# Kernel optimization log

Hardware: AMD Instinct MI355X
Metric: run time of the kernel (lower is better)

## Reference

```python
import jax, jax.numpy as jnp
import numpy as np

N, E, D = 40000, 640000, 128
BN_EPS = 1e-5


def setup_inputs() -> dict:
    key = jax.random.key(0)
    ks = jax.random.split(key, 6)
    x = jax.random.normal(ks[0], (N, D), dtype=jnp.float32)
    src = jax.random.randint(ks[1], (E,), 0, N, dtype=jnp.int64)
    dst = jax.random.randint(ks[2], (E,), 0, N, dtype=jnp.int64)
    W1 = jax.random.normal(ks[3], (D, D), dtype=jnp.float32) * (1.0 / np.sqrt(D))
    b1 = jnp.zeros((D,), dtype=jnp.float32)
    gamma = jnp.ones((D,), dtype=jnp.float32)
    beta = jnp.zeros((D,), dtype=jnp.float32)
    W2 = jax.random.normal(ks[4], (D, D), dtype=jnp.float32) * (1.0 / np.sqrt(D))
    b2 = jnp.zeros((D,), dtype=jnp.float32)
    eps = jnp.zeros((1,), dtype=jnp.float32)
    return {"x": x, "src": src, "dst": dst, "W1": W1, "b1": b1,
            "gamma": gamma, "beta": beta, "W2": W2, "b2": b2, "eps": eps}


def reference(x, src, dst, W1, b1, gamma, beta, W2, b2, eps):
    # edge gather + ReLU + scatter-sum aggregation  (copy_u -> relu -> sum)
    m = jax.nn.relu(x[src])                                  # [E, D]
    agg = jax.ops.segment_sum(m, dst, num_segments=N)        # [N, D]
    h = (1.0 + eps[0]) * x + agg                             # eps-scaled residual
    # MLP: Linear -> BatchNorm1d (batch stats) -> ReLU -> Linear
    h = h @ W1.T + b1
    mu = jnp.mean(h, axis=0)
    var = jnp.var(h, axis=0)                                 # biased, as torch BN
    h = (h - mu) * jax.lax.rsqrt(var + BN_EPS) * gamma + beta
    h = jax.nn.relu(h)
    return h @ W2.T + b2
```

## Files before the change

kernel.cpp:

```cpp
#include <hip/hip_runtime.h>

#define NN 40000
#define NE 640000
#define DD 128
#define CAP 64
#define NREP 8
#define NBLK 625
#define PA_BLOCKS 512
#define EPB (NE / PA_BLOCKS)
#define NBUCK 256
#define NODES_PB 157
#define CELL 32

typedef __attribute__((ext_vector_type(8))) short short8;
typedef __attribute__((ext_vector_type(4))) float floatx4;

__device__ __forceinline__ unsigned short f2bf(float f) {
    union { float f; unsigned u; } v; v.f = f;
    return (unsigned short)((v.u + 0x7fffu + ((v.u >> 16) & 1u)) >> 16);
}
__device__ __forceinline__ float bflo2f(unsigned u) {
    union { unsigned u; float f; } v; v.u = u << 16; return v.f;
}
__device__ __forceinline__ float bfhi2f(unsigned u) {
    union { unsigned u; float f; } v; v.u = u & 0xffff0000u; return v.f;
}


__global__ void k_passA(const int* __restrict__ src, const int* __restrict__ dst,
                        const float* __restrict__ x, const float* __restrict__ W1,
                        const float* __restrict__ W2, unsigned* __restrict__ part,
                        unsigned char* __restrict__ cntAB, unsigned short* __restrict__ xb,
                        unsigned short* __restrict__ W1b, unsigned short* __restrict__ W2b,
                        float* __restrict__ stats) {
    __shared__ unsigned hist[NBUCK];
    const int t = threadIdx.x, k = blockIdx.x;
    if (k == 0) {
        float4 z = {0.f, 0.f, 0.f, 0.f};
        ((float4*)stats)[t * 2] = z;
        ((float4*)stats)[t * 2 + 1] = z;
    }
    if (t < NBUCK) hist[t] = 0;
    __syncthreads();
    const int base = k * EPB;
    unsigned* myWin = part + ((unsigned)k << 8) * CELL;
    for (int i = t; i < EPB; i += 256) {
        int sv = src[base + i];
        int d  = dst[base + i];
        unsigned b = (unsigned)d / NODES_PB;
        unsigned slot = atomicAdd(&hist[b], 1u);
        if (slot < CELL)
            myWin[b * CELL + slot] =
                ((unsigned)(d - (int)(b * NODES_PB)) << 16) | (unsigned)sv;
    }
    __syncthreads();
    if (t < NBUCK) {
        unsigned c = hist[t];
        cntAB[k * NBUCK + t] = (unsigned char)(c < CELL ? c : CELL);
    }
    const int tid = k * 256 + t;
    const int P = PA_BLOCKS * 256;
    const float4* x4 = (const float4*)x;
    for (int i = tid; i < NN * DD / 4; i += P) {
        float4 v = x4[i];
        ushort4 o;
        o.x = f2bf(v.x); o.y = f2bf(v.y); o.z = f2bf(v.z); o.w = f2bf(v.w);
        ((ushort4*)xb)[i] = o;
    }
    if (tid < 8192) {
        const float4* w4 = (tid < 4096) ? (const float4*)W1 : (const float4*)W2;
        unsigned short* wb = (tid < 4096) ? W1b : W2b;
        int i = tid & 4095;
        float4 v = w4[i];
        ushort4 o;
        o.x = f2bf(v.x); o.y = f2bf(v.y); o.z = f2bf(v.z); o.w = f2bf(v.w);
        ((ushort4*)wb)[i] = o;
    }
}

__launch_bounds__(256)
__global__ void k_passB(const unsigned* __restrict__ part,
                        const unsigned char* __restrict__ cntAB,
                        int* __restrict__ cnt, unsigned short* __restrict__ eidx) {
    __shared__ unsigned lcnt[NODES_PB];
    __shared__ __align__(16) unsigned short llist[NODES_PB][CAP];
    const int g = blockIdx.x;
    const int t = threadIdx.x;
    const int n0 = g * NODES_PB;
    const int nCnt = (NN - n0 < NODES_PB) ? (NN - n0) : NODES_PB;
    if (t < NODES_PB) lcnt[t] = 0;
    __syncthreads();
    for (int k = t; k < PA_BLOCKS; k += 256) {
        int c = cntAB[k * NBUCK + g];
        const unsigned* cell = part + (((unsigned)k << 8) | (unsigned)g) * CELL;
        for (int i = 0; i < c; ++i) {
            unsigned e = cell[i];
            unsigned d = e >> 16;
            unsigned slot = atomicAdd(&lcnt[d], 1u);
            if (slot < CAP) llist[d][slot] = (unsigned short)(e & 0xffffu);
        }
    }
    __syncthreads();
    if (t < nCnt) cnt[n0 + t] = (int)lcnt[t];
    for (int idx = t; idx < nCnt * 8; idx += 256) {
        int row = idx >> 3, c = idx & 7;
        unsigned lc = lcnt[row]; lc = (lc > CAP) ? CAP : lc;
        if ((unsigned)c * 8 < lc)
            ((uint4*)eidx)[(unsigned)(n0 + row) * 8 + c] = *(const uint4*)&llist[row][c * 8];
    }
}

__launch_bounds__(256)
__global__ void k_gather(const unsigned short* __restrict__ xb,
                         const unsigned short* __restrict__ eidx,
                         const int* __restrict__ cnt, const float* __restrict__ eps,
                         unsigned short* __restrict__ h) {
    const int n = blockIdx.x * 4 + (threadIdx.x >> 6);
    const int lane = threadIdx.x & 63;
    const int half = lane >> 5, hl = lane & 31;
    const float s = 1.0f + eps[0];
    const uint2* xq = (const uint2*)xb;
    int deg = cnt[n];
    deg = (deg > CAP) ? CAP : deg;
    float f0, f1, f2, f3;
    {
        uint2 xv = xq[n * 32 + hl];
        float sm = (half == 0) ? s : 0.f;
        f0 = bflo2f(xv.x) * sm; f1 = bfhi2f(xv.x) * sm;
        f2 = bflo2f(xv.y) * sm; f3 = bfhi2f(xv.y) * sm;
    }
    const unsigned short* row = eidx + n * CAP;
    int j = 0;
    for (; j + 15 < deg; j += 16) {
        int e0 = row[j + half],      e1 = row[j + 2 + half];
        int e2 = row[j + 4 + half],  e3 = row[j + 6 + half];
        int e4 = row[j + 8 + half],  e5 = row[j + 10 + half];
        int e6 = row[j + 12 + half], e7 = row[j + 14 + half];
        uint2 v0 = xq[e0 * 32 + hl];
        uint2 v1 = xq[e1 * 32 + hl];
        uint2 v2 = xq[e2 * 32 + hl];
        uint2 v3 = xq[e3 * 32 + hl];
        uint2 v4 = xq[e4 * 32 + hl];
        uint2 v5 = xq[e5 * 32 + hl];
        uint2 v6 = xq[e6 * 32 + hl];
        uint2 v7 = xq[e7 * 32 + hl];
        f0 += ((fmaxf(bflo2f(v0.x), 0.f) + fmaxf(bflo2f(v1.x), 0.f)) +
               (fmaxf(bflo2f(v2.x), 0.f) + fmaxf(bflo2f(v3.x), 0.f))) +
              ((fmaxf(bflo2f(v4.x), 0.f) + fmaxf(bflo2f(v5.x), 0.f)) +
               (fmaxf(bflo2f(v6.x), 0.f) + fmaxf(bflo2f(v7.x), 0.f)));
        f1 += ((fmaxf(bfhi2f(v0.x), 0.f) + fmaxf(bfhi2f(v1.x), 0.f)) +
               (fmaxf(bfhi2f(v2.x), 0.f) + fmaxf(bfhi2f(v3.x), 0.f))) +
              ((fmaxf(bfhi2f(v4.x), 0.f) + fmaxf(bfhi2f(v5.x), 0.f)) +
               (fmaxf(bfhi2f(v6.x), 0.f) + fmaxf(bfhi2f(v7.x), 0.f)));
        f2 += ((fmaxf(bflo2f(v0.y), 0.f) + fmaxf(bflo2f(v1.y), 0.f)) +
               (fmaxf(bflo2f(v2.y), 0.f) + fmaxf(bflo2f(v3.y), 0.f))) +
              ((fmaxf(bflo2f(v4.y), 0.f) + fmaxf(bflo2f(v5.y), 0.f)) +
               (fmaxf(bflo2f(v6.y), 0.f) + fmaxf(bflo2f(v7.y), 0.f)));
        f3 += ((fmaxf(bfhi2f(v0.y), 0.f) + fmaxf(bfhi2f(v1.y), 0.f)) +
               (fmaxf(bfhi2f(v2.y), 0.f) + fmaxf(bfhi2f(v3.y), 0.f))) +
              ((fmaxf(bfhi2f(v4.y), 0.f) + fmaxf(bfhi2f(v5.y), 0.f)) +
               (fmaxf(bfhi2f(v6.y), 0.f) + fmaxf(bfhi2f(v7.y), 0.f)));
    }
    for (; j + 7 < deg; j += 8) {
        int e0 = row[j + half],     e1 = row[j + 2 + half];
        int e2 = row[j + 4 + half], e3 = row[j + 6 + half];
        uint2 v0 = xq[e0 * 32 + hl];
        uint2 v1 = xq[e1 * 32 + hl];
        uint2 v2 = xq[e2 * 32 + hl];
        uint2 v3 = xq[e3 * 32 + hl];
        f0 += (fmaxf(bflo2f(v0.x), 0.f) + fmaxf(bflo2f(v1.x), 0.f)) +
              (fmaxf(bflo2f(v2.x), 0.f) + fmaxf(bflo2f(v3.x), 0.f));
        f1 += (fmaxf(bfhi2f(v0.x), 0.f) + fmaxf(bfhi2f(v1.x), 0.f)) +
              (fmaxf(bfhi2f(v2.x), 0.f) + fmaxf(bfhi2f(v3.x), 0.f));
        f2 += (fmaxf(bflo2f(v0.y), 0.f) + fmaxf(bflo2f(v1.y), 0.f)) +
              (fmaxf(bflo2f(v2.y), 0.f) + fmaxf(bflo2f(v3.y), 0.f));
        f3 += (fmaxf(bfhi2f(v0.y), 0.f) + fmaxf(bfhi2f(v1.y), 0.f)) +
              (fmaxf(bfhi2f(v2.y), 0.f) + fmaxf(bfhi2f(v3.y), 0.f));
    }
    for (; j + 1 < deg; j += 2) {
        int e = row[j + half];
        uint2 v = xq[e * 32 + hl];
        f0 += fmaxf(bflo2f(v.x), 0.f); f1 += fmaxf(bfhi2f(v.x), 0.f);
        f2 += fmaxf(bflo2f(v.y), 0.f); f3 += fmaxf(bfhi2f(v.y), 0.f);
    }
    if (j < deg && half == 0) {
        int e = row[j];
        uint2 v = xq[e * 32 + hl];
        f0 += fmaxf(bflo2f(v.x), 0.f); f1 += fmaxf(bfhi2f(v.x), 0.f);
        f2 += fmaxf(bflo2f(v.y), 0.f); f3 += fmaxf(bfhi2f(v.y), 0.f);
    }
    f0 += __shfl_xor(f0, 32); f1 += __shfl_xor(f1, 32);
    f2 += __shfl_xor(f2, 32); f3 += __shfl_xor(f3, 32);
    if (half == 0) {
        unsigned lo = ((unsigned)f2bf(f1) << 16) | (unsigned)f2bf(f0);
        unsigned hi = ((unsigned)f2bf(f3) << 16) | (unsigned)f2bf(f2);
        ((uint2*)h)[n * 32 + hl] = make_uint2(lo, hi);
    }
}

__launch_bounds__(256)
__global__ void k_gg1(const unsigned short* __restrict__ h,
                      const unsigned short* __restrict__ W1b, const float* __restrict__ b1,
                      unsigned short* __restrict__ h1b, float* __restrict__ stats) {
    __shared__ __align__(16) unsigned short hbuf[64][DD + 8];
    __shared__ float red[2][4][DD];
    const int t = threadIdx.x;
    const int wv = t >> 6, lane = t & 63, m = lane & 15, q = lane >> 4;
    const int r0 = blockIdx.x * 64 + wv * 16;
    floatx4 acc[8];
    #pragma unroll
    for (int nt = 0; nt < 8; ++nt) acc[nt] = (floatx4){0.f, 0.f, 0.f, 0.f};
    {
        const unsigned short* arow = h + (r0 + m) * DD + q * 8;
        const unsigned short* brow = W1b + m * DD + q * 8;
        #pragma unroll
        for (int kt = 0; kt < 4; ++kt) {
            short8 a = *(const short8*)(arow + kt * 32);
            #pragma unroll
            for (int nt = 0; nt < 8; ++nt) {
                short8 b = *(const short8*)(brow + nt * 16 * DD + kt * 32);
                acc[nt] = __builtin_amdgcn_mfma_f32_16x16x32_bf16(a, b, acc[nt], 0, 0, 0);
            }
        }
    }
    #pragma unroll
    for (int nt = 0; nt < 8; ++nt) {
        float bv = b1[nt * 16 + m];
        float cs = 0.f, cq = 0.f;
        #pragma unroll
        for (int r = 0; r < 4; ++r) {
            float v = acc[nt][r] + bv;
            acc[nt][r] = v;
            cs += v;
            cq = fmaf(v, v, cq);
        }
        cs += __shfl_xor(cs, 16); cs += __shfl_xor(cs, 32);
        cq += __shfl_xor(cq, 16); cq += __shfl_xor(cq, 32);
        if (q == 0) { red[0][wv][nt * 16 + m] = cs; red[1][wv][nt * 16 + m] = cq; }
    }
    __syncthreads();
    {
        int plane = t >> 7, jj = t & 127;
        float v = (red[plane][0][jj] + red[plane][1][jj]) + (red[plane][2][jj] + red[plane][3][jj]);
        atomicAdd(stats + (blockIdx.x & (NREP - 1)) * 256 + plane * DD + jj, v);
    }
    #pragma unroll
    for (int nt = 0; nt < 8; ++nt) {
        const int col = nt * 16 + m;
        #pragma unroll
        for (int r = 0; r < 4; ++r)
            hbuf[wv * 16 + q * 4 + r][col] = f2bf(acc[nt][r]);
    }
    __syncthreads();
    {
        uint4* dst4 = (uint4*)h1b + blockIdx.x * 1024;
        #pragma unroll
        for (int i = 0; i < 4; ++i) {
            int c = t + 256 * i;
            int rr = c >> 4, cc = c & 15;
            dst4[c] = *(const uint4*)&hbuf[rr][cc * 8];
        }
    }
}

__launch_bounds__(256)
__global__ void k_gemm2(const unsigned short* __restrict__ h1b,
                        const unsigned short* __restrict__ W2b,
                        const float* __restrict__ b2, const float* __restrict__ stats,
                        const float* __restrict__ gamma, const float* __restrict__ beta,
                        float* __restrict__ out) {
    __shared__ float ssc[DD], ssh[DD];
    const int t = threadIdx.x;
    if (t < DD) {
        float s0 = 0.f, s1 = 0.f;
        #pragma unroll
        for (int rp = 0; rp < NREP; ++rp) {
            s0 += stats[rp * 256 + t];
            s1 += stats[rp * 256 + DD + t];
        }
        const float inv_n = 1.0f / (float)NN;
        float mu = s0 * inv_n;
        float var = s1 * inv_n - mu * mu;
        float sc = rsqrtf(var + 1e-5f) * gamma[t];
        ssc[t] = sc;
        ssh[t] = beta[t] - mu * sc;
    }
    __syncthreads();
    const int wv = t >> 6, lane = t & 63, m = lane & 15, q = lane >> 4;
    const int r0 = blockIdx.x * 64 + wv * 16;
    floatx4 acc[8];
    #pragma unroll
    for (int nt = 0; nt < 8; ++nt) acc[nt] = (floatx4){0.f, 0.f, 0.f, 0.f};
    const unsigned short* arow = h1b + (r0 + m) * DD + q * 8;
    const unsigned short* brow = W2b + m * DD + q * 8;
    #pragma unroll
    for (int kt = 0; kt < 4; ++kt) {
        uint4 w = *(const uint4*)(arow + kt * 32);
        const int k0 = kt * 32 + q * 8;
        float4 c0 = *(const float4*)(ssc + k0);
        float4 c1 = *(const float4*)(ssc + k0 + 4);
        float4 d0 = *(const float4*)(ssh + k0);
        float4 d1 = *(const float4*)(ssh + k0 + 4);
        short8 a;
        a[0] = (short)f2bf(fmaxf(fmaf(bflo2f(w.x), c0.x, d0.x), 0.f));
        a[1] = (short)f2bf(fmaxf(fmaf(bfhi2f(w.x), c0.y, d0.y), 0.f));
        a[2] = (short)f2bf(fmaxf(fmaf(bflo2f(w.y), c0.z, d0.z), 0.f));
        a[3] = (short)f2bf(fmaxf(fmaf(bfhi2f(w.y), c0.w, d0.w), 0.f));
        a[4] = (short)f2bf(fmaxf(fmaf(bflo2f(w.z), c1.x, d1.x), 0.f));
        a[5] = (short)f2bf(fmaxf(fmaf(bfhi2f(w.z), c1.y, d1.y), 0.f));
        a[6] = (short)f2bf(fmaxf(fmaf(bflo2f(w.w), c1.z, d1.z), 0.f));
        a[7] = (short)f2bf(fmaxf(fmaf(bfhi2f(w.w), c1.w, d1.w), 0.f));
        #pragma unroll
        for (int nt = 0; nt < 8; ++nt) {
            short8 b = *(const short8*)(brow + nt * 16 * DD + kt * 32);
            acc[nt] = __builtin_amdgcn_mfma_f32_16x16x32_bf16(a, b, acc[nt], 0, 0, 0);
        }
    }
    #pragma unroll
    for (int nt = 0; nt < 8; ++nt) {
        float bv = b2[nt * 16 + m];
        #pragma unroll
        for (int r = 0; r < 4; ++r)
            out[(r0 + q * 4 + r) * DD + nt * 16 + m] = acc[nt][r] + bv;
    }
}

extern "C" void kernel_launch(void* const* d_in, const int* in_sizes, int n_in,
                              void* d_out, int out_size, void* d_ws, size_t ws_size,
                              hipStream_t stream) {
    const float* x     = (const float*)d_in[0];
    const int*   src   = (const int*)d_in[1];
    const int*   dst   = (const int*)d_in[2];
    const float* W1    = (const float*)d_in[3];
    const float* b1    = (const float*)d_in[4];
    const float* gamma = (const float*)d_in[5];
    const float* beta  = (const float*)d_in[6];
    const float* W2    = (const float*)d_in[7];
    const float* b2    = (const float*)d_in[8];
    const float* eps   = (const float*)d_in[9];
    float* out = (float*)d_out;

    unsigned short* xb  = (unsigned short*)d_ws;
    unsigned short* h   = xb + NN * DD;
    unsigned short* h1b = h + NN * DD;
    unsigned short* W1b = h1b + NN * DD;
    unsigned short* W2b = W1b + DD * DD;
    float* stats = (float*)(W2b + DD * DD);
    int*   cnt   = (int*)(stats + NREP * 256);
    unsigned short* eidx = (unsigned short*)(cnt + NN);
    unsigned* part = (unsigned*)(eidx + NN * CAP);
    unsigned char* cntAB = (unsigned char*)(part + PA_BLOCKS * NBUCK * CELL);

    hipLaunchKernelGGL(k_passA, dim3(PA_BLOCKS), dim3(256), 0, stream,
                       src, dst, x, W1, W2, part, cntAB, xb, W1b, W2b, stats);
    hipLaunchKernelGGL(k_passB, dim3(255), dim3(256), 0, stream,
                       part, cntAB, cnt, eidx);
    hipLaunchKernelGGL(k_gather, dim3(NN / 4), dim3(256), 0, stream,
                       xb, eidx, cnt, eps, h);
    hipLaunchKernelGGL(k_gg1,    dim3(NBLK), dim3(256), 0, stream,
                       h, W1b, b1, h1b, stats);
    hipLaunchKernelGGL(k_gemm2,  dim3(NBLK), dim3(256), 0, stream,
                       h1b, W2b, b2, stats, gamma, beta, out);
}
```

Baseline: 165.4 us.

## Recompute first GEMM in second kernel and widen gather loads to 16 bytes

The first-GEMM kernel now only computes the batch-norm column statistics and no longer writes the intermediate h1 to memory. The second kernel recomputes h@W1 from h, applies the BN affine and ReLU, stages the result as bf16 in shared memory and runs the second GEMM. This trades a redundant MFMA GEMM for skipping a 10 MB intermediate write and read. Separately, the gather kernel switches to 16-byte loads with four edges per wave step, cutting per-edge load instructions at the cost of more cross-lane shuffles.

```diff
diff --git a/kernel.cpp b/kernel.cpp
--- a/kernel.cpp
+++ b/kernel.cpp
@@ -24,6 +24,9 @@
 }
 __device__ __forceinline__ float bfhi2f(unsigned u) {
     union { unsigned u; float f; } v; v.u = u & 0xffff0000u; return v.f;
+}
+__device__ __forceinline__ unsigned packbf(float lo, float hi) {
+    return ((unsigned)f2bf(hi) << 16) | (unsigned)f2bf(lo);
 }
 
 
@@ -117,94 +120,133 @@
                          unsigned short* __restrict__ h) {
     const int n = blockIdx.x * 4 + (threadIdx.x >> 6);
     const int lane = threadIdx.x & 63;
-    const int half = lane >> 5, hl = lane & 31;
+    const int qw = lane >> 4, ql = lane & 15;
     const float s = 1.0f + eps[0];
-    const uint2* xq = (const uint2*)xb;
+    const uint4* xq = (const uint4*)xb;
     int deg = cnt[n];
     deg = (deg > CAP) ? CAP : deg;
-    float f0, f1, f2, f3;
+    float f0, f1, f2, f3, f4, f5, f6, f7;
     {
-        uint2 xv = xq[n * 32 + hl];
-        float sm = (half == 0) ? s : 0.f;
+        uint4 xv = xq[n * 16 + ql];
+        float sm = (qw == 0) ? s : 0.f;
         f0 = bflo2f(xv.x) * sm; f1 = bfhi2f(xv.x) * sm;
         f2 = bflo2f(xv.y) * sm; f3 = bfhi2f(xv.y) * sm;
+        f4 = bflo2f(xv.z) * sm; f5 = bfhi2f(xv.z) * sm;
+        f6 = bflo2f(xv.w) * sm; f7 = bfhi2f(xv.w) * sm;
     }
     const unsigned short* row = eidx + n * CAP;
     int j = 0;
+#define ACC8(v) \
+    f0 += fmaxf(bflo2f((v).x), 0.f); f1 += fmaxf(bfhi2f((v).x), 0.f); \
+    f2 += fmaxf(bflo2f((v).y), 0.f); f3 += fmaxf(bfhi2f((v).y), 0.f); \
+    f4 += fmaxf(bflo2f((v).z), 0.f); f5 += fmaxf(bfhi2f((v).z), 0.f); \
+    f6 += fmaxf(bflo2f((v).w), 0.f); f7 += fmaxf(bfhi2f((v).w), 0.f);
     for (; j + 15 < deg; j += 16) {
-        int e0 = row[j + half],      e1 = row[j + 2 + half];
-        int e2 = row[j + 4 + half],  e3 = row[j + 6 + half];
-        int e4 = row[j + 8 + half],  e5 = row[j + 10 + half];
-        int e6 = row[j + 12 + half], e7 = row[j + 14 + half];
-        uint2 v0 = xq[e0 * 32 + hl];
-        uint2 v1 = xq[e1 * 32 + hl];
-        uint2 v2 = xq[e2 * 32 + hl];
-        uint2 v3 = xq[e3 * 32 + hl];
-        uint2 v4 = xq[e4 * 32 + hl];
-        uint2 v5 = xq[e5 * 32 + hl];
-        uint2 v6 = xq[e6 * 32 + hl];
-        uint2 v7 = xq[e7 * 32 + hl];
-        f0 += ((fmaxf(bflo2f(v0.x), 0.f) + fmaxf(bflo2f(v1.x), 0.f)) +
-               (fmaxf(bflo2f(v2.x), 0.f) + fmaxf(bflo2f(v3.x), 0.f))) +
-              ((fmaxf(bflo2f(v4.x), 0.f) + fmaxf(bflo2f(v5.x), 0.f)) +
-               (fmaxf(bflo2f(v6.x), 0.f) + fmaxf(bflo2f(v7.x), 0.f)));
-        f1 += ((fmaxf(bfhi2f(v0.x), 0.f) + fmaxf(bfhi2f(v1.x), 0.f)) +
-               (fmaxf(bfhi2f(v2.x), 0.f) + fmaxf(bfhi2f(v3.x), 0.f))) +
-              ((fmaxf(bfhi2f(v4.x), 0.f) + fmaxf(bfhi2f(v5.x), 0.f)) +
-               (fmaxf(bfhi2f(v6.x), 0.f) + fmaxf(bfhi2f(v7.x), 0.f)));
-        f2 += ((fmaxf(bflo2f(v0.y), 0.f) + fmaxf(bflo2f(v1.y), 0.f)) +
-               (fmaxf(bflo2f(v2.y), 0.f) + fmaxf(bflo2f(v3.y), 0.f))) +
-              ((fmaxf(bflo2f(v4.y), 0.f) + fmaxf(bflo2f(v5.y), 0.f)) +
-               (fmaxf(bflo2f(v6.y), 0.f) + fmaxf(bflo2f(v7.y), 0.f)));
-        f3 += ((fmaxf(bfhi2f(v0.y), 0.f) + fmaxf(bfhi2f(v1.y), 0.f)) +
-               (fmaxf(bfhi2f(v2.y), 0.f) + fmaxf(bfhi2f(v3.y), 0.f))) +
-              ((fmaxf(bfhi2f(v4.y), 0.f) + fmaxf(bfhi2f(v5.y), 0.f)) +
-               (fmaxf(bfhi2f(v6.y), 0.f) + fmaxf(bfhi2f(v7.y), 0.f)));
-    }
-    for (; j + 7 < deg; j += 8) {
-        int e0 = row[j + half],     e1 = row[j + 2 + half];
-        int e2 = row[j + 4 + half], e3 = row[j + 6 + half];
-        uint2 v0 = xq[e0 * 32 + hl];
-        uint2 v1 = xq[e1 * 32 + hl];
-        uint2 v2 = xq[e2 * 32 + hl];
-        uint2 v3 = xq[e3 * 32 + hl];
-        f0 += (fmaxf(bflo2f(v0.x), 0.f) + fmaxf(bflo2f(v1.x), 0.f)) +
-              (fmaxf(bflo2f(v2.x), 0.f) + fmaxf(bflo2f(v3.x), 0.f));
-        f1 += (fmaxf(bfhi2f(v0.x), 0.f) + fmaxf(bfhi2f(v1.x), 0.f)) +
-              (fmaxf(bfhi2f(v2.x), 0.f) + fmaxf(bfhi2f(v3.x), 0.f));
-        f2 += (fmaxf(bflo2f(v0.y), 0.f) + fmaxf(bflo2f(v1.y), 0.f)) +
-              (fmaxf(bflo2f(v2.y), 0.f) + fmaxf(bflo2f(v3.y), 0.f));
-        f3 += (fmaxf(bfhi2f(v0.y), 0.f) + fmaxf(bfhi2f(v1.y), 0.f)) +
-              (fmaxf(bfhi2f(v2.y), 0.f) + fmaxf(bfhi2f(v3.y), 0.f));
-    }
-    for (; j + 1 < deg; j += 2) {
-        int e = row[j + half];
-        uint2 v = xq[e * 32 + hl];
-        f0 += fmaxf(bflo2f(v.x), 0.f); f1 += fmaxf(bfhi2f(v.x), 0.f);
-        f2 += fmaxf(bflo2f(v.y), 0.f); f3 += fmaxf(bfhi2f(v.y), 0.f);
-    }
-    if (j < deg && half == 0) {
-        int e = row[j];
-        uint2 v = xq[e * 32 + hl];
-        f0 += fmaxf(bflo2f(v.x), 0.f); f1 += fmaxf(bfhi2f(v.x), 0.f);
-        f2 += fmaxf(bflo2f(v.y), 0.f); f3 += fmaxf(bfhi2f(v.y), 0.f);
-    }
-    f0 += __shfl_xor(f0, 32); f1 += __shfl_xor(f1, 32);
-    f2 += __shfl_xor(f2, 32); f3 += __shfl_xor(f3, 32);
-    if (half == 0) {
-        unsigned lo = ((unsigned)f2bf(f1) << 16) | (unsigned)f2bf(f0);
-        unsigned hi = ((unsigned)f2bf(f3) << 16) | (unsigned)f2bf(f2);
-        ((uint2*)h)[n * 32 + hl] = make_uint2(lo, hi);
+        int e0 = row[j + qw],      e1 = row[j + 4 + qw];
+        int e2 = row[j + 8 + qw],  e3 = row[j + 12 + qw];
+        uint4 v0 = xq[e0 * 16 + ql];
+        uint4 v1 = xq[e1 * 16 + ql];
+        uint4 v2 = xq[e2 * 16 + ql];
+        uint4 v3 = xq[e3 * 16 + ql];
+        ACC8(v0) ACC8(v1) ACC8(v2) ACC8(v3)
+    }
+    for (; j + 3 < deg; j += 4) {
+        int e = row[j + qw];
+        uint4 v = xq[e * 16 + ql];
+        ACC8(v)
+    }
+    if (j < deg && qw < deg - j) {
+        int e = row[j + qw];
+        uint4 v = xq[e * 16 + ql];
+        ACC8(v)
+    }
+#undef ACC8
+    f0 += __shfl_xor(f0, 16); f0 += __shfl_xor(f0, 32);
+    f1 += __shfl_xor(f1, 16); f1 += __shfl_xor(f1, 32);
+    f2 += __shfl_xor(f2, 16); f2 += __shfl_xor(f2, 32);
+    f3 += __shfl_xor(f3, 16); f3 += __shfl_xor(f3, 32);
+    f4 += __shfl_xor(f4, 16); f4 += __shfl_xor(f4, 32);
+    f5 += __shfl_xor(f5, 16); f5 += __shfl_xor(f5, 32);
+    f6 += __shfl_xor(f6, 16); f6 += __shfl_xor(f6, 32);
+    f7 += __shfl_xor(f7, 16); f7 += __shfl_xor(f7, 32);
+    if (qw == 0) {
+        uint4 o;
+        o.x = packbf(f0, f1); o.y = packbf(f2, f3);
+        o.z = packbf(f4, f5); o.w = packbf(f6, f7);
+        ((uint4*)h)[n * 16 + ql] = o;
     }
 }
 
 __launch_bounds__(256)
-__global__ void k_gg1(const unsigned short* __restrict__ h,
-                      const unsigned short* __restrict__ W1b, const float* __restrict__ b1,
-                      unsigned short* __restrict__ h1b, float* __restrict__ stats) {
-    __shared__ __align__(16) unsigned short hbuf[64][DD + 8];
+__global__ void k_gg1s(const unsigned short* __restrict__ h,
+                       const unsigned short* __restrict__ W1b,
+                       const float* __restrict__ b1, float* __restrict__ stats) {
     __shared__ float red[2][4][DD];
     const int t = threadIdx.x;
+    const int wv = t >> 6, lane = t & 63, m = lane & 15, q = lane >> 4;
+    const int r0 = blockIdx.x * 64 + wv * 16;
+    floatx4 acc[8];
+    #pragma unroll
+    for (int nt = 0; nt < 8; ++nt) acc[nt] = (floatx4){0.f, 0.f, 0.f, 0.f};
+    const unsigned short* arow = h + (r0 + m) * DD + q * 8;
+    const unsigned short* brow = W1b + m * DD + q * 8;
+    #pragma unroll
+    for (int kt = 0; kt < 4; ++kt) {
+        short8 a = *(const short8*)(arow + kt * 32);
+        #pragma unroll
+        for (int nt = 0; nt < 8; ++nt) {
+            short8 b = *(const short8*)(brow + nt * 16 * DD + kt * 32);
+            acc[nt] = __builtin_amdgcn_mfma_f32_16x16x32_bf16(a, b, acc[nt], 0, 0, 0);
+        }
+    }
+    #pragma unroll
+    for (int nt = 0; nt < 8; ++nt) {
+        float bv = b1[nt * 16 + m];
+        float cs = 0.f, cq = 0.f;
+        #pragma unroll
+        for (int r = 0; r < 4; ++r) {
+            float v = acc[nt][r] + bv;
+            cs += v;
+            cq = fmaf(v, v, cq);
+        }
+        cs += __shfl_xor(cs, 16); cs += __shfl_xor(cs, 32);
+        cq += __shfl_xor(cq, 16); cq += __shfl_xor(cq, 32);
+        if (q == 0) { red[0][wv][nt * 16 + m] = cs; red[1][wv][nt * 16 + m] = cq; }
+    }
+    __syncthreads();
+    {
+        int plane = t >> 7, jj = t & 127;
+        float v = (red[plane][0][jj] + red[plane][1][jj]) + (red[plane][2][jj] + red[plane][3][jj]);
+        atomicAdd(stats + (blockIdx.x & (NREP - 1)) * 256 + plane * DD + jj, v);
+    }
+}
+
+__launch_bounds__(256)
+__global__ void k_gemm2(const unsigned short* __restrict__ h,
+                        const unsigned short* __restrict__ W1b,
+                        const unsigned short* __restrict__ W2b,
+                        const float* __restrict__ b1, const float* __restrict__ b2,
+                        const float* __restrict__ stats,
+                        const float* __restrict__ gamma, const float* __restrict__ beta,
+                        float* __restrict__ out) {
+    __shared__ float ssc[DD], ssh[DD];
+    __shared__ __align__(16) unsigned short a2[64][DD + 8];
+    const int t = threadIdx.x;
+    if (t < DD) {
+        float s0 = 0.f, s1 = 0.f;
+        #pragma unroll
+        for (int rp = 0; rp < NREP; ++rp) {
+            s0 += stats[rp * 256 + t];
+            s1 += stats[rp * 256 + DD + t];
+        }
+        const float inv_n = 1.0f / (float)NN;
+        float mu = s0 * inv_n;
+        float var = s1 * inv_n - mu * mu;
+        float sc = rsqrtf(var + 1e-5f) * gamma[t];
+        ssc[t] = sc;
+        ssh[t] = beta[t] - mu * sc;
+    }
+    __syncthreads();
     const int wv = t >> 6, lane = t & 63, m = lane & 15, q = lane >> 4;
     const int r0 = blockIdx.x * 64 + wv * 16;
     floatx4 acc[8];
@@ -225,95 +267,29 @@
     }
     #pragma unroll
     for (int nt = 0; nt < 8; ++nt) {
-        float bv = b1[nt * 16 + m];
-        float cs = 0.f, cq = 0.f;
+        const int col = nt * 16 + m;
+        float bv = b1[col];
+        float sc = ssc[col], shv = ssh[col];
         #pragma unroll
         for (int r = 0; r < 4; ++r) {
-            float v = acc[nt][r] + bv;
-            acc[nt][r] = v;
-            cs += v;
-            cq = fmaf(v, v, cq);
-        }
-        cs += __shfl_xor(cs, 16); cs += __shfl_xor(cs, 32);
-        cq += __shfl_xor(cq, 16); cq += __shfl_xor(cq, 32);
-        if (q == 0) { red[0][wv][nt * 16 + m] = cs; red[1][wv][nt * 16 + m] = cq; }
-    }
-    __syncthreads();
+            float v = fmaxf(fmaf(acc[nt][r] + bv, sc, shv), 0.f);
+            a2[wv * 16 + q * 4 + r][col] = f2bf(v);
+        }
+    }
+    __syncthreads();
+    floatx4 acc2[8];
+    #pragma unroll
+    for (int nt = 0; nt < 8; ++nt) acc2[nt] = (floatx4){0.f, 0.f, 0.f, 0.f};
     {
-        int plane = t >> 7, jj = t & 127;
-        float v = (red[plane][0][jj] + red[plane][1][jj]) + (red[plane][2][jj] + red[plane][3][jj]);
-        atomicAdd(stats + (blockIdx.x & (NREP - 1)) * 256 + plane * DD + jj, v);
-    }
-    #pragma unroll
-    for (int nt = 0; nt < 8; ++nt) {
-        const int col = nt * 16 + m;
-        #pragma unroll
-        for (int r = 0; r < 4; ++r)
-            hbuf[wv * 16 + q * 4 + r][col] = f2bf(acc[nt][r]);
-    }
-    __syncthreads();
-    {
-        uint4* dst4 = (uint4*)h1b + blockIdx.x * 1024;
-        #pragma unroll
-        for (int i = 0; i < 4; ++i) {
-            int c = t + 256 * i;
-            int rr = c >> 4, cc = c & 15;
-            dst4[c] = *(const uint4*)&hbuf[rr][cc * 8];
-        }
-    }
-}
-
-__launch_bounds__(256)
-__global__ void k_gemm2(const unsigned short* __restrict__ h1b,
-                        const unsigned short* __restrict__ W2b,
-                        const float* __restrict__ b2, const float* __restrict__ stats,
-                        const float* __restrict__ gamma, const float* __restrict__ beta,
-                        float* __restrict__ out) {
-    __shared__ float ssc[DD], ssh[DD];
-    const int t = threadIdx.x;
-    if (t < DD) {
-        float s0 = 0.f, s1 = 0.f;
-        #pragma unroll
-        for (int rp = 0; rp < NREP; ++rp) {
-            s0 += stats[rp * 256 + t];
-            s1 += stats[rp * 256 + DD + t];
-        }
-        const float inv_n = 1.0f / (float)NN;
-        float mu = s0 * inv_n;
-        float var = s1 * inv_n - mu * mu;
-        float sc = rsqrtf(var + 1e-5f) * gamma[t];
-        ssc[t] = sc;
-        ssh[t] = beta[t] - mu * sc;
-    }
-    __syncthreads();
-    const int wv = t >> 6, lane = t & 63, m = lane & 15, q = lane >> 4;
-    const int r0 = blockIdx.x * 64 + wv * 16;
-    floatx4 acc[8];
-    #pragma unroll
-    for (int nt = 0; nt < 8; ++nt) acc[nt] = (floatx4){0.f, 0.f, 0.f, 0.f};
-    const unsigned short* arow = h1b + (r0 + m) * DD + q * 8;
-    const unsigned short* brow = W2b + m * DD + q * 8;
-    #pragma unroll
-    for (int kt = 0; kt < 4; ++kt) {
-        uint4 w = *(const uint4*)(arow + kt * 32);
-        const int k0 = kt * 32 + q * 8;
-        float4 c0 = *(const float4*)(ssc + k0);
-        float4 c1 = *(const float4*)(ssc + k0 + 4);
-        float4 d0 = *(const float4*)(ssh + k0);
-        float4 d1 = *(const float4*)(ssh + k0 + 4);
-        short8 a;
-        a[0] = (short)f2bf(fmaxf(fmaf(bflo2f(w.x), c0.x, d0.x), 0.f));
-        a[1] = (short)f2bf(fmaxf(fmaf(bfhi2f(w.x), c0.y, d0.y), 0.f));
-        a[2] = (short)f2bf(fmaxf(fmaf(bflo2f(w.y), c0.z, d0.z), 0.f));
-        a[3] = (short)f2bf(fmaxf(fmaf(bfhi2f(w.y), c0.w, d0.w), 0.f));
-        a[4] = (short)f2bf(fmaxf(fmaf(bflo2f(w.z), c1.x, d1.x), 0.f));
-        a[5] = (short)f2bf(fmaxf(fmaf(bfhi2f(w.z), c1.y, d1.y), 0.f));
-        a[6] = (short)f2bf(fmaxf(fmaf(bflo2f(w.w), c1.z, d1.z), 0.f));
-        a[7] = (short)f2bf(fmaxf(fmaf(bfhi2f(w.w), c1.w, d1.w), 0.f));
-        #pragma unroll
-        for (int nt = 0; nt < 8; ++nt) {
-            short8 b = *(const short8*)(brow + nt * 16 * DD + kt * 32);
-            acc[nt] = __builtin_amdgcn_mfma_f32_16x16x32_bf16(a, b, acc[nt], 0, 0, 0);
+        const unsigned short* brow = W2b + m * DD + q * 8;
+        #pragma unroll
+        for (int kt = 0; kt < 4; ++kt) {
+            short8 a = *(const short8*)&a2[wv * 16 + m][q * 8 + kt * 32];
+            #pragma unroll
+            for (int nt = 0; nt < 8; ++nt) {
+                short8 b = *(const short8*)(brow + nt * 16 * DD + kt * 32);
+                acc2[nt] = __builtin_amdgcn_mfma_f32_16x16x32_bf16(a, b, acc2[nt], 0, 0, 0);
+            }
         }
     }
     #pragma unroll
@@ -321,7 +297,7 @@
         float bv = b2[nt * 16 + m];
         #pragma unroll
         for (int r = 0; r < 4; ++r)
-            out[(r0 + q * 4 + r) * DD + nt * 16 + m] = acc[nt][r] + bv;
+            out[(r0 + q * 4 + r) * DD + nt * 16 + m] = acc2[nt][r] + bv;
     }
 }
 
@@ -342,8 +318,7 @@
 
     unsigned short* xb  = (unsigned short*)d_ws;
     unsigned short* h   = xb + NN * DD;
-    unsigned short* h1b = h + NN * DD;
-    unsigned short* W1b = h1b + NN * DD;
+    unsigned short* W1b = h + NN * DD;
     unsigned short* W2b = W1b + DD * DD;
     float* stats = (float*)(W2b + DD * DD);
     int*   cnt   = (int*)(stats + NREP * 256);
@@ -357,8 +332,8 @@
                        part, cntAB, cnt, eidx);
     hipLaunchKernelGGL(k_gather, dim3(NN / 4), dim3(256), 0, stream,
                        xb, eidx, cnt, eps, h);
-    hipLaunchKernelGGL(k_gg1,    dim3(NBLK), dim3(256), 0, stream,
-                       h, W1b, b1, h1b, stats);
-    hipLaunchKernelGGL(k_gemm2,  dim3(NBLK), dim3(256), 0, stream,
-                       h1b, W2b, b2, stats, gamma, beta, out);
-}
+    hipLaunchKernelGGL(k_gg1s,  dim3(NBLK), dim3(256), 0, stream,
+                       h, W1b, b1, stats);
+    hipLaunchKernelGGL(k_gemm2, dim3(NBLK), dim3(256), 0, stream,
+                       h, W1b, W2b, b1, b2, stats, gamma, beta, out);
+}
```

Result: slower. 176.2 us (+6.6%).

## Fuse both MLP GEMMs into one kernel with a grid-wide barrier for BN stats

Applied to the files above, without the earlier changes.

Merges the first GEMM with the BatchNorm statistics and the second GEMM into a single persistent-style kernel. An atomic counter acts as a grid barrier, so every block waits until all batch statistics are accumulated before normalizing its tile held in LDS. This removes the bf16 h1 round trip through global memory and one kernel launch. It relies on all 625 blocks being co-resident (launch bounds of 3 blocks per CU) and accepts the cost of spin-waiting and possible deadlock if they are not.

```diff
diff --git a/kernel.cpp b/kernel.cpp
--- a/kernel.cpp
+++ b/kernel.cpp
@@ -32,13 +32,15 @@
                         const float* __restrict__ W2, unsigned* __restrict__ part,
                         unsigned char* __restrict__ cntAB, unsigned short* __restrict__ xb,
                         unsigned short* __restrict__ W1b, unsigned short* __restrict__ W2b,
-                        float* __restrict__ stats) {
+                        float* __restrict__ stats, int* __restrict__ done) {
     __shared__ unsigned hist[NBUCK];
     const int t = threadIdx.x, k = blockIdx.x;
     if (k == 0) {
         float4 z = {0.f, 0.f, 0.f, 0.f};
         ((float4*)stats)[t * 2] = z;
         ((float4*)stats)[t * 2 + 1] = z;
+        if (t == 0)
+            __hip_atomic_store(done, 0, __ATOMIC_RELAXED, __HIP_MEMORY_SCOPE_AGENT);
     }
     if (t < NBUCK) hist[t] = 0;
     __syncthreads();
@@ -198,15 +200,21 @@
     }
 }
 
-__launch_bounds__(256)
-__global__ void k_gg1(const unsigned short* __restrict__ h,
-                      const unsigned short* __restrict__ W1b, const float* __restrict__ b1,
-                      unsigned short* __restrict__ h1b, float* __restrict__ stats) {
+__launch_bounds__(256, 3)
+__global__ void k_mlp(const unsigned short* __restrict__ h,
+                      const unsigned short* __restrict__ W1b,
+                      const unsigned short* __restrict__ W2b,
+                      const float* __restrict__ b1, const float* __restrict__ b2,
+                      const float* __restrict__ gamma, const float* __restrict__ beta,
+                      float* __restrict__ stats, int* __restrict__ done,
+                      float* __restrict__ out) {
     __shared__ __align__(16) unsigned short hbuf[64][DD + 8];
     __shared__ float red[2][4][DD];
+    __shared__ float ssc[DD], ssh[DD];
     const int t = threadIdx.x;
     const int wv = t >> 6, lane = t & 63, m = lane & 15, q = lane >> 4;
     const int r0 = blockIdx.x * 64 + wv * 16;
+
     floatx4 acc[8];
     #pragma unroll
     for (int nt = 0; nt < 8; ++nt) acc[nt] = (floatx4){0.f, 0.f, 0.f, 0.f};
@@ -244,39 +252,21 @@
         float v = (red[plane][0][jj] + red[plane][1][jj]) + (red[plane][2][jj] + red[plane][3][jj]);
         atomicAdd(stats + (blockIdx.x & (NREP - 1)) * 256 + plane * DD + jj, v);
     }
-    #pragma unroll
-    for (int nt = 0; nt < 8; ++nt) {
-        const int col = nt * 16 + m;
-        #pragma unroll
-        for (int r = 0; r < 4; ++r)
-            hbuf[wv * 16 + q * 4 + r][col] = f2bf(acc[nt][r]);
-    }
-    __syncthreads();
-    {
-        uint4* dst4 = (uint4*)h1b + blockIdx.x * 1024;
-        #pragma unroll
-        for (int i = 0; i < 4; ++i) {
-            int c = t + 256 * i;
-            int rr = c >> 4, cc = c & 15;
-            dst4[c] = *(const uint4*)&hbuf[rr][cc * 8];
-        }
-    }
-}
-
-__launch_bounds__(256)
-__global__ void k_gemm2(const unsigned short* __restrict__ h1b,
-                        const unsigned short* __restrict__ W2b,
-                        const float* __restrict__ b2, const float* __restrict__ stats,
-                        const float* __restrict__ gamma, const float* __restrict__ beta,
-                        float* __restrict__ out) {
-    __shared__ float ssc[DD], ssh[DD];
-    const int t = threadIdx.x;
+    __syncthreads();
+    if (t == 0) {
+        __hip_atomic_fetch_add(done, 1, __ATOMIC_ACQ_REL, __HIP_MEMORY_SCOPE_AGENT);
+        while (__hip_atomic_load(done, __ATOMIC_ACQUIRE, __HIP_MEMORY_SCOPE_AGENT) < NBLK)
+            __builtin_amdgcn_s_sleep(8);
+    }
+    __syncthreads();
     if (t < DD) {
         float s0 = 0.f, s1 = 0.f;
         #pragma unroll
         for (int rp = 0; rp < NREP; ++rp) {
-            s0 += stats[rp * 256 + t];
-            s1 += stats[rp * 256 + DD + t];
+            s0 += __hip_atomic_load(&stats[rp * 256 + t], __ATOMIC_RELAXED,
+                                    __HIP_MEMORY_SCOPE_AGENT);
+            s1 += __hip_atomic_load(&stats[rp * 256 + DD + t], __ATOMIC_RELAXED,
+                                    __HIP_MEMORY_SCOPE_AGENT);
         }
         const float inv_n = 1.0f / (float)NN;
         float mu = s0 * inv_n;
@@ -286,34 +276,30 @@
         ssh[t] = beta[t] - mu * sc;
     }
     __syncthreads();
-    const int wv = t >> 6, lane = t & 63, m = lane & 15, q = lane >> 4;
-    const int r0 = blockIdx.x * 64 + wv * 16;
-    floatx4 acc[8];
-    #pragma unroll
-    for (int nt = 0; nt < 8; ++nt) acc[nt] = (floatx4){0.f, 0.f, 0.f, 0.f};
-    const unsigned short* arow = h1b + (r0 + m) * DD + q * 8;
-    const unsigned short* brow = W2b + m * DD + q * 8;
-    #pragma unroll
-    for (int kt = 0; kt < 4; ++kt) {
-        uint4 w = *(const uint4*)(arow + kt * 32);
-        const int k0 = kt * 32 + q * 8;
-        float4 c0 = *(const float4*)(ssc + k0);
-        float4 c1 = *(const float4*)(ssc + k0 + 4);
-        float4 d0 = *(const float4*)(ssh + k0);
-        float4 d1 = *(const float4*)(ssh + k0 + 4);
-        short8 a;
-        a[0] = (short)f2bf(fmaxf(fmaf(bflo2f(w.x), c0.x, d0.x), 0.f));
-        a[1] = (short)f2bf(fmaxf(fmaf(bfhi2f(w.x), c0.y, d0.y), 0.f));
-        a[2] = (short)f2bf(fmaxf(fmaf(bflo2f(w.y), c0.z, d0.z), 0.f));
-        a[3] = (short)f2bf(fmaxf(fmaf(bfhi2f(w.y), c0.w, d0.w), 0.f));
-        a[4] = (short)f2bf(fmaxf(fmaf(bflo2f(w.z), c1.x, d1.x), 0.f));
-        a[5] = (short)f2bf(fmaxf(fmaf(bfhi2f(w.z), c1.y, d1.y), 0.f));
-        a[6] = (short)f2bf(fmaxf(fmaf(bflo2f(w.w), c1.z, d1.z), 0.f));
-        a[7] = (short)f2bf(fmaxf(fmaf(bfhi2f(w.w), c1.w, d1.w), 0.f));
-        #pragma unroll
-        for (int nt = 0; nt < 8; ++nt) {
-            short8 b = *(const short8*)(brow + nt * 16 * DD + kt * 32);
-            acc[nt] = __builtin_amdgcn_mfma_f32_16x16x32_bf16(a, b, acc[nt], 0, 0, 0);
+    #pragma unroll
+    for (int nt = 0; nt < 8; ++nt) {
+        const int col = nt * 16 + m;
+        float sc = ssc[col], shv = ssh[col];
+        #pragma unroll
+        for (int r = 0; r < 4; ++r) {
+            float v = fmaxf(fmaf(acc[nt][r], sc, shv), 0.f);
+            hbuf[wv * 16 + q * 4 + r][col] = f2bf(v);
+        }
+    }
+    __syncthreads();
+    floatx4 acc2[8];
+    #pragma unroll
+    for (int nt = 0; nt < 8; ++nt) acc2[nt] = (floatx4){0.f, 0.f, 0.f, 0.f};
+    {
+        const unsigned short* brow = W2b + m * DD + q * 8;
+        #pragma unroll
+        for (int kt = 0; kt < 4; ++kt) {
+            short8 a = *(const short8*)&hbuf[wv * 16 + m][q * 8 + kt * 32];
+            #pragma unroll
+            for (int nt = 0; nt < 8; ++nt) {
+                short8 b = *(const short8*)(brow + nt * 16 * DD + kt * 32);
+                acc2[nt] = __builtin_amdgcn_mfma_f32_16x16x32_bf16(a, b, acc2[nt], 0, 0, 0);
+            }
         }
     }
     #pragma unroll
@@ -321,7 +307,7 @@
         float bv = b2[nt * 16 + m];
         #pragma unroll
         for (int r = 0; r < 4; ++r)
-            out[(r0 + q * 4 + r) * DD + nt * 16 + m] = acc[nt][r] + bv;
+            out[(r0 + q * 4 + r) * DD + nt * 16 + m] = acc2[nt][r] + bv;
     }
 }
 
@@ -342,23 +328,21 @@
 
     unsigned short* xb  = (unsigned short*)d_ws;
     unsigned short* h   = xb + NN * DD;
-    unsigned short* h1b = h + NN * DD;
-    unsigned short* W1b = h1b + NN * DD;
+    unsigned short* W1b = h + NN * DD;
     unsigned short* W2b = W1b + DD * DD;
     float* stats = (float*)(W2b + DD * DD);
-    int*   cnt   = (int*)(stats + NREP * 256);
+    int*   done  = (int*)(stats + NREP * 256);
+    int*   cnt   = done + 16;
     unsigned short* eidx = (unsigned short*)(cnt + NN);
     unsigned* part = (unsigned*)(eidx + NN * CAP);
     unsigned char* cntAB = (unsigned char*)(part + PA_BLOCKS * NBUCK * CELL);
 
     hipLaunchKernelGGL(k_passA, dim3(PA_BLOCKS), dim3(256), 0, stream,
-                       src, dst, x, W1, W2, part, cntAB, xb, W1b, W2b, stats);
+                       src, dst, x, W1, W2, part, cntAB, xb, W1b, W2b, stats, done);
     hipLaunchKernelGGL(k_passB, dim3(255), dim3(256), 0, stream,
                        part, cntAB, cnt, eidx);
     hipLaunchKernelGGL(k_gather, dim3(NN / 4), dim3(256), 0, stream,
                        xb, eidx, cnt, eps, h);
-    hipLaunchKernelGGL(k_gg1,    dim3(NBLK), dim3(256), 0, stream,
-                       h, W1b, b1, h1b, stats);
-    hipLaunchKernelGGL(k_gemm2,  dim3(NBLK), dim3(256), 0, stream,
-                       h1b, W2b, b2, stats, gamma, beta, out);
-}
+    hipLaunchKernelGGL(k_mlp,   dim3(NBLK), dim3(256), 0, stream,
+                       h, W1b, W2b, b1, b2, gamma, beta, stats, done, out);
+}
```

After: 196.5 us. 18.8% more time.
